# Kernel tuning notes

Hardware: AMD Instinct MI355X
Metric: run time of the kernel (lower is better)

## Reference

```python
import jax, jax.numpy as jnp
import numpy as np

# (multiplicity, irrep_dim) for irreps_in == irreps_out: 128x0e + 64x1o + 32x2e
IRREPS = [(128, 1), (64, 3), (32, 5)]
NUM_INDICES = 64
N_ELEMENTS = 8192
SCALE = 1.0  # module's `scale` arg; total coeff = scale / sqrt(num_indices) / sqrt(mul_in)
W_DIM = sum(m * m for m, _ in IRREPS)  # 21504


def setup_inputs() -> dict:
    key = jax.random.key(0)
    ks = jax.random.split(key, 5)
    x0 = jax.random.normal(ks[0], (N_ELEMENTS, 128, 1), jnp.float32)
    x1 = jax.random.normal(ks[1], (N_ELEMENTS, 64, 3), jnp.float32)
    x2 = jax.random.normal(ks[2], (N_ELEMENTS, 32, 5), jnp.float32)
    w = jax.random.normal(ks[3], (NUM_INDICES, W_DIM), jnp.float32)
    # Random contiguous segment sizes that sum exactly to N_ELEMENTS:
    bnd = jnp.sort(jax.random.randint(ks[4], (NUM_INDICES - 1,), 0, N_ELEMENTS + 1)).astype(jnp.int32)
    counts = jnp.diff(jnp.concatenate([jnp.zeros((1,), jnp.int32), bnd,
                                       jnp.full((1,), N_ELEMENTS, jnp.int32)]))
    return {"x0": x0, "x1": x1, "x2": x2, "w": w, "num_index_counts": counts}


def reference(x0, x1, x2, w, num_index_counts):
    """Indexed (segmented) equivariant linear: rows are grouped contiguously by
    num_index_counts; segment g uses weight row w[g]. Per matched irrep the
    weight block is a (mul_in, mul_out) mixing matrix applied identically to
    each of the ir.dim components (Schur's lemma), with fan-in normalization
    1/sqrt(mul_in) (cue.descriptors.linear) times scale/sqrt(num_indices)."""
    n = x0.shape[0]
    # segment id per row (rows are already grouped contiguously, as in Repeats())
    sid = jnp.repeat(jnp.arange(NUM_INDICES), num_index_counts, total_repeat_length=n)
    xs = (x0, x1, x2)
    ys = []
    off = 0
    for xk, (mul, ir_dim) in zip(xs, IRREPS):
        blk = w[:, off:off + mul * mul].reshape(NUM_INDICES, mul, mul)  # (E, m_in, m_out)
        coeff = float(SCALE / np.sqrt(NUM_INDICES) / np.sqrt(mul))
        wk = blk[sid]  # (n, m_in, m_out) per-row weight gather
        # y[n, o, i] = coeff * sum_m x[n, m, i] * w[g(n), m, o]
        ys.append(coeff * jnp.einsum('nmi,nmo->noi', xk, wk))
        off += mul * mul
    return tuple(ys)
```

## Files before the change

### kernel.cpp

```cpp
#include <hip/hip_runtime.h>

#define NSEG 64
#define NROW 8192
#define WROW 21504
#define NBPP 576
#define T0   32
#define T12  16
#define PX0  132
#define P1   196
#define P2   164
#define SBUF_FLOATS 4224

__global__ __launch_bounds__(256) void iil_kernel(
    const float* __restrict__ x0, const float* __restrict__ x1, const float* __restrict__ x2,
    const float* __restrict__ w, const int* __restrict__ counts,
    float* __restrict__ y0, float* __restrict__ y1, float* __restrict__ y2)
{
    __shared__ float sbuf[SBUF_FLOATS];
    __shared__ int sstart[NSEG + 1];
    __shared__ int t16s[NSEG + 1];
    __shared__ int t32s[NSEG + 1];

    const int t = threadIdx.x;

    if (t < NSEG) {
        int c = counts[t];
        int v = c;
        #pragma unroll
        for (int d = 1; d < NSEG; d <<= 1) {
            int u = __shfl_up(v, d, 64);
            if (t >= d) v += u;
        }
        sstart[t + 1] = v;
        int a = (c + 15) >> 4;
        #pragma unroll
        for (int d = 1; d < NSEG; d <<= 1) {
            int u = __shfl_up(a, d, 64);
            if (t >= d) a += u;
        }
        t16s[t + 1] = a;
        int b2 = (c + 31) >> 5;
        #pragma unroll
        for (int d = 1; d < NSEG; d <<= 1) {
            int u = __shfl_up(b2, d, 64);
            if (t >= d) b2 += u;
        }
        t32s[t + 1] = b2;
        if (t == 0) { sstart[0] = 0; t16s[0] = 0; t32s[0] = 0; }
    }
    __syncthreads();

    const int phase = blockIdx.x / NBPP;
    const int pb = blockIdx.x - phase * NBPP;
    const float4 z4 = make_float4(0.f, 0.f, 0.f, 0.f);

    if (phase == 0) {
        if (pb >= t32s[NSEG]) return;
        int lo = 0, hi = NSEG;
        while (hi - lo > 1) {
            int mid = (lo + hi) >> 1;
            if (t32s[mid] <= pb) lo = mid; else hi = mid;
        }
        const int g = lo;
        const int s = sstart[g] + (pb - t32s[g]) * T0;
        const int nr = min(T0, sstart[g + 1] - s);
        const float* __restrict__ wseg = w + (size_t)g * WROW;

        const float4* g0 = (const float4*)x0 + (size_t)s * 32;
        #pragma unroll
        for (int i = 0; i < 4; ++i) {
            int idx = t + i * 256;
            int r = idx >> 5, c4 = idx & 31;
            float4 v = (r < nr) ? g0[idx] : z4;
            *(float4*)(sbuf + r * PX0 + c4 * 4) = v;
        }
        __syncthreads();

        const int og = t & 31;
        const int rg = t >> 5;
        const float* wp = wseg + og * 4;
        const float* xb = sbuf + rg * 4 * PX0;
        float acc[16];
        #pragma unroll
        for (int i = 0; i < 16; ++i) acc[i] = 0.f;

        #pragma unroll 2
        for (int kq = 0; kq < 32; ++kq) {
            const int k = kq * 4;
            float4 xq0 = *(const float4*)(xb + 0 * PX0 + k);
            float4 xq1 = *(const float4*)(xb + 1 * PX0 + k);
            float4 xq2 = *(const float4*)(xb + 2 * PX0 + k);
            float4 xq3 = *(const float4*)(xb + 3 * PX0 + k);
            float4 w0q = *(const float4*)(wp + (size_t)(k + 0) * 128);
            float4 w1q = *(const float4*)(wp + (size_t)(k + 1) * 128);
            float4 w2q = *(const float4*)(wp + (size_t)(k + 2) * 128);
            float4 w3q = *(const float4*)(wp + (size_t)(k + 3) * 128);
#define RF(J, XQ)                                              \
            acc[J*4+0] = fmaf(XQ.x, w0q.x, acc[J*4+0]);        \
            acc[J*4+1] = fmaf(XQ.x, w0q.y, acc[J*4+1]);        \
            acc[J*4+2] = fmaf(XQ.x, w0q.z, acc[J*4+2]);        \
            acc[J*4+3] = fmaf(XQ.x, w0q.w, acc[J*4+3]);        \
            acc[J*4+0] = fmaf(XQ.y, w1q.x, acc[J*4+0]);        \
            acc[J*4+1] = fmaf(XQ.y, w1q.y, acc[J*4+1]);        \
            acc[J*4+2] = fmaf(XQ.y, w1q.z, acc[J*4+2]);        \
            acc[J*4+3] = fmaf(XQ.y, w1q.w, acc[J*4+3]);        \
            acc[J*4+0] = fmaf(XQ.z, w2q.x, acc[J*4+0]);        \
            acc[J*4+1] = fmaf(XQ.z, w2q.y, acc[J*4+1]);        \
            acc[J*4+2] = fmaf(XQ.z, w2q.z, acc[J*4+2]);        \
            acc[J*4+3] = fmaf(XQ.z, w2q.w, acc[J*4+3]);        \
            acc[J*4+0] = fmaf(XQ.w, w3q.x, acc[J*4+0]);        \
            acc[J*4+1] = fmaf(XQ.w, w3q.y, acc[J*4+1]);        \
            acc[J*4+2] = fmaf(XQ.w, w3q.z, acc[J*4+2]);        \
            acc[J*4+3] = fmaf(XQ.w, w3q.w, acc[J*4+3]);
            RF(0, xq0)
            RF(1, xq1)
            RF(2, xq2)
            RF(3, xq3)
#undef RF
        }
        const float c0 = 0.011048543456039806f;
        #pragma unroll
        for (int j = 0; j < 4; ++j) {
            int r = rg * 4 + j;
            if (r < nr) {
                *(float4*)(y0 + (size_t)(s + r) * 128 + og * 4) =
                    make_float4(acc[j*4+0] * c0, acc[j*4+1] * c0,
                                acc[j*4+2] * c0, acc[j*4+3] * c0);
            }
        }
    } else if (phase == 1) {
        if (pb >= t16s[NSEG]) return;
        int lo = 0, hi = NSEG;
        while (hi - lo > 1) {
            int mid = (lo + hi) >> 1;
            if (t16s[mid] <= pb) lo = mid; else hi = mid;
        }
        const int g = lo;
        const int s = sstart[g] + (pb - t16s[g]) * T12;
        const int nr = min(T12, sstart[g + 1] - s);
        const float* __restrict__ wseg = w + (size_t)g * WROW;

        float* sx1 = sbuf;
        const float4* g1 = (const float4*)x1 + (size_t)s * 48;
        #pragma unroll
        for (int i = 0; i < 3; ++i) {
            int idx = t + i * 256;
            int r = idx / 48, c = idx - r * 48;
            float4 v = (r < nr) ? g1[idx] : z4;
            *(float4*)(sx1 + r * P1 + c * 4) = v;
        }
        __syncthreads();

        const int og = t & 15;
        const int r = t >> 4;
        const float* xrow = sx1 + r * P1;
        const float* wp = wseg + 16384 + og * 4;
        float acc[12];
        #pragma unroll
        for (int i = 0; i < 12; ++i) acc[i] = 0.f;
        #pragma unroll 2
        for (int kq = 0; kq < 16; ++kq) {
            float4 xq0 = *(const float4*)(xrow + 12 * kq + 0);
            float4 xq1 = *(const float4*)(xrow + 12 * kq + 4);
            float4 xq2 = *(const float4*)(xrow + 12 * kq + 8);
            float xf[12] = {xq0.x, xq0.y, xq0.z, xq0.w,
                            xq1.x, xq1.y, xq1.z, xq1.w,
                            xq2.x, xq2.y, xq2.z, xq2.w};
            #pragma unroll
            for (int kk = 0; kk < 4; ++kk) {
                float4 wv = *(const float4*)(wp + (size_t)(4 * kq + kk) * 64);
                #pragma unroll
                for (int oo = 0; oo < 4; ++oo) {
                    float wvo = (oo == 0) ? wv.x : (oo == 1) ? wv.y : (oo == 2) ? wv.z : wv.w;
                    acc[oo * 3 + 0] = fmaf(wvo, xf[kk * 3 + 0], acc[oo * 3 + 0]);
                    acc[oo * 3 + 1] = fmaf(wvo, xf[kk * 3 + 1], acc[oo * 3 + 1]);
                    acc[oo * 3 + 2] = fmaf(wvo, xf[kk * 3 + 2], acc[oo * 3 + 2]);
                }
            }
        }
        const float c1 = 0.015625f;
        if (r < nr) {
            float* yb = y1 + (size_t)(s + r) * 192 + og * 12;
            *(float4*)(yb + 0) = make_float4(acc[0] * c1, acc[1] * c1, acc[2] * c1, acc[3] * c1);
            *(float4*)(yb + 4) = make_float4(acc[4] * c1, acc[5] * c1, acc[6] * c1, acc[7] * c1);
            *(float4*)(yb + 8) = make_float4(acc[8] * c1, acc[9] * c1, acc[10] * c1, acc[11] * c1);
        }
    } else {
        if (pb >= t16s[NSEG]) return;
        int lo = 0, hi = NSEG;
        while (hi - lo > 1) {
            int mid = (lo + hi) >> 1;
            if (t16s[mid] <= pb) lo = mid; else hi = mid;
        }
        const int g = lo;
        const int s = sstart[g] + (pb - t16s[g]) * T12;
        const int nr = min(T12, sstart[g + 1] - s);
        const float* __restrict__ wseg = w + (size_t)g * WROW;

        float* sx2 = sbuf;
        const float4* g2 = (const float4*)x2 + (size_t)s * 40;
        #pragma unroll
        for (int i = 0; i < 3; ++i) {
            int idx = t + i * 256;
            if (idx < 640) {
                int r = idx / 40, c = idx - r * 40;
                float4 v = (r < nr) ? g2[idx] : z4;
                *(float4*)(sx2 + r * P2 + c * 4) = v;
            }
        }
        __syncthreads();

        const int og = t & 15;
        const int r = t >> 4;
        const float* xrow = sx2 + r * P2;
        const float* wp = wseg + 20480 + og * 2;
        float acc[10];
        #pragma unroll
        for (int i = 0; i < 10; ++i) acc[i] = 0.f;
        #pragma unroll
        for (int kq = 0; kq < 8; ++kq) {
            float xf[20];
            #pragma unroll
            for (int j = 0; j < 5; ++j) {
                float4 v = *(const float4*)(xrow + 20 * kq + 4 * j);
                xf[4 * j + 0] = v.x; xf[4 * j + 1] = v.y; xf[4 * j + 2] = v.z; xf[4 * j + 3] = v.w;
            }
            #pragma unroll
            for (int kk = 0; kk < 4; ++kk) {
                float2 wv = *(const float2*)(wp + (size_t)(4 * kq + kk) * 32);
                #pragma unroll
                for (int i = 0; i < 5; ++i) {
                    acc[i]     = fmaf(wv.x, xf[5 * kk + i], acc[i]);
                    acc[5 + i] = fmaf(wv.y, xf[5 * kk + i], acc[5 + i]);
                }
            }
        }
        const float c2 = 0.022097086912079608f;
        if (r < nr) {
            float* yb = y2 + (size_t)(s + r) * 160 + og * 10;
            #pragma unroll
            for (int i = 0; i < 5; ++i)
                *(float2*)(yb + 2 * i) = make_float2(acc[2 * i] * c2, acc[2 * i + 1] * c2);
        }
    }
}

extern "C" void kernel_launch(void* const* d_in, const int* in_sizes, int n_in,
                              void* d_out, int out_size, void* d_ws, size_t ws_size,
                              hipStream_t stream) {
    const float* x0 = (const float*)d_in[0];
    const float* x1 = (const float*)d_in[1];
    const float* x2 = (const float*)d_in[2];
    const float* w  = (const float*)d_in[3];
    const int* counts = (const int*)d_in[4];

    float* y0 = (float*)d_out;
    float* y1 = y0 + (size_t)NROW * 128;
    float* y2 = y1 + (size_t)NROW * 192;

    hipLaunchKernelGGL(iil_kernel, dim3(3 * NBPP), dim3(256), 0, stream,
                       x0, x1, x2, w, counts, y0, y1, y2);
}
```

Measured before the change: 90.85 us.

## Software-pipeline weight loads, interleave phase blocks, set occupancy launch bound

Each phase's inner product loop now double-buffers weight (and for phase 0, shared-memory x) loads in registers, issuing the next step's global loads before computing the current step to hide latency. Block-to-phase mapping changes from contiguous ranges to round-robin (blockIdx % 3) so heavy and light phases mix across CUs. Launch bounds now request 4 blocks per SM, which may cap registers and risk spills given the doubled register buffers.

```diff
diff --git a/kernel.cpp b/kernel.cpp
--- a/kernel.cpp
+++ b/kernel.cpp
@@ -11,7 +11,7 @@
 #define P2   164
 #define SBUF_FLOATS 4224
 
-__global__ __launch_bounds__(256) void iil_kernel(
+__global__ __launch_bounds__(256, 4) void iil_kernel(
     const float* __restrict__ x0, const float* __restrict__ x1, const float* __restrict__ x2,
     const float* __restrict__ w, const int* __restrict__ counts,
     float* __restrict__ y0, float* __restrict__ y1, float* __restrict__ y2)
@@ -50,8 +50,8 @@
     }
     __syncthreads();
 
-    const int phase = blockIdx.x / NBPP;
-    const int pb = blockIdx.x - phase * NBPP;
+    const int phase = blockIdx.x % 3;
+    const int pb = blockIdx.x / 3;
     const float4 z4 = make_float4(0.f, 0.f, 0.f, 0.f);
 
     if (phase == 0) {
@@ -84,40 +84,51 @@
         #pragma unroll
         for (int i = 0; i < 16; ++i) acc[i] = 0.f;
 
-        #pragma unroll 2
-        for (int kq = 0; kq < 32; ++kq) {
-            const int k = kq * 4;
-            float4 xq0 = *(const float4*)(xb + 0 * PX0 + k);
-            float4 xq1 = *(const float4*)(xb + 1 * PX0 + k);
-            float4 xq2 = *(const float4*)(xb + 2 * PX0 + k);
-            float4 xq3 = *(const float4*)(xb + 3 * PX0 + k);
-            float4 w0q = *(const float4*)(wp + (size_t)(k + 0) * 128);
-            float4 w1q = *(const float4*)(wp + (size_t)(k + 1) * 128);
-            float4 w2q = *(const float4*)(wp + (size_t)(k + 2) * 128);
-            float4 w3q = *(const float4*)(wp + (size_t)(k + 3) * 128);
-#define RF(J, XQ)                                              \
-            acc[J*4+0] = fmaf(XQ.x, w0q.x, acc[J*4+0]);        \
-            acc[J*4+1] = fmaf(XQ.x, w0q.y, acc[J*4+1]);        \
-            acc[J*4+2] = fmaf(XQ.x, w0q.z, acc[J*4+2]);        \
-            acc[J*4+3] = fmaf(XQ.x, w0q.w, acc[J*4+3]);        \
-            acc[J*4+0] = fmaf(XQ.y, w1q.x, acc[J*4+0]);        \
-            acc[J*4+1] = fmaf(XQ.y, w1q.y, acc[J*4+1]);        \
-            acc[J*4+2] = fmaf(XQ.y, w1q.z, acc[J*4+2]);        \
-            acc[J*4+3] = fmaf(XQ.y, w1q.w, acc[J*4+3]);        \
-            acc[J*4+0] = fmaf(XQ.z, w2q.x, acc[J*4+0]);        \
-            acc[J*4+1] = fmaf(XQ.z, w2q.y, acc[J*4+1]);        \
-            acc[J*4+2] = fmaf(XQ.z, w2q.z, acc[J*4+2]);        \
-            acc[J*4+3] = fmaf(XQ.z, w2q.w, acc[J*4+3]);        \
-            acc[J*4+0] = fmaf(XQ.w, w3q.x, acc[J*4+0]);        \
-            acc[J*4+1] = fmaf(XQ.w, w3q.y, acc[J*4+1]);        \
-            acc[J*4+2] = fmaf(XQ.w, w3q.z, acc[J*4+2]);        \
-            acc[J*4+3] = fmaf(XQ.w, w3q.w, acc[J*4+3]);
-            RF(0, xq0)
-            RF(1, xq1)
-            RF(2, xq2)
-            RF(3, xq3)
-#undef RF
-        }
+        float4 wA[4], xA[4], wB[4], xB[4];
+#define LD0(WQ, XQ, KQ) do {                                      \
+            const int k_ = (KQ) * 4;                              \
+            WQ[0] = *(const float4*)(wp + (size_t)(k_ + 0) * 128);\
+            WQ[1] = *(const float4*)(wp + (size_t)(k_ + 1) * 128);\
+            WQ[2] = *(const float4*)(wp + (size_t)(k_ + 2) * 128);\
+            WQ[3] = *(const float4*)(wp + (size_t)(k_ + 3) * 128);\
+            XQ[0] = *(const float4*)(xb + 0 * PX0 + k_);          \
+            XQ[1] = *(const float4*)(xb + 1 * PX0 + k_);          \
+            XQ[2] = *(const float4*)(xb + 2 * PX0 + k_);          \
+            XQ[3] = *(const float4*)(xb + 3 * PX0 + k_);          \
+        } while (0)
+#define RF0(J, XV, WQ)                                         \
+            acc[J*4+0] = fmaf(XV.x, WQ[0].x, acc[J*4+0]);      \
+            acc[J*4+1] = fmaf(XV.x, WQ[0].y, acc[J*4+1]);      \
+            acc[J*4+2] = fmaf(XV.x, WQ[0].z, acc[J*4+2]);      \
+            acc[J*4+3] = fmaf(XV.x, WQ[0].w, acc[J*4+3]);      \
+            acc[J*4+0] = fmaf(XV.y, WQ[1].x, acc[J*4+0]);      \
+            acc[J*4+1] = fmaf(XV.y, WQ[1].y, acc[J*4+1]);      \
+            acc[J*4+2] = fmaf(XV.y, WQ[1].z, acc[J*4+2]);      \
+            acc[J*4+3] = fmaf(XV.y, WQ[1].w, acc[J*4+3]);      \
+            acc[J*4+0] = fmaf(XV.z, WQ[2].x, acc[J*4+0]);      \
+            acc[J*4+1] = fmaf(XV.z, WQ[2].y, acc[J*4+1]);      \
+            acc[J*4+2] = fmaf(XV.z, WQ[2].z, acc[J*4+2]);      \
+            acc[J*4+3] = fmaf(XV.z, WQ[2].w, acc[J*4+3]);      \
+            acc[J*4+0] = fmaf(XV.w, WQ[3].x, acc[J*4+0]);      \
+            acc[J*4+1] = fmaf(XV.w, WQ[3].y, acc[J*4+1]);      \
+            acc[J*4+2] = fmaf(XV.w, WQ[3].z, acc[J*4+2]);      \
+            acc[J*4+3] = fmaf(XV.w, WQ[3].w, acc[J*4+3]);
+#define CP0(WQ, XQ) { RF0(0, XQ[0], WQ) RF0(1, XQ[1], WQ) RF0(2, XQ[2], WQ) RF0(3, XQ[3], WQ) }
+
+        LD0(wA, xA, 0);
+        LD0(wB, xB, 1);
+        #pragma unroll 1
+        for (int kq = 0; kq < 30; kq += 2) {
+            CP0(wA, xA);
+            LD0(wA, xA, kq + 2);
+            CP0(wB, xB);
+            LD0(wB, xB, kq + 3);
+        }
+        CP0(wA, xA);
+        CP0(wB, xB);
+#undef LD0
+#undef RF0
+#undef CP0
         const float c0 = 0.011048543456039806f;
         #pragma unroll
         for (int j = 0; j < 4; ++j) {
@@ -158,26 +169,52 @@
         float acc[12];
         #pragma unroll
         for (int i = 0; i < 12; ++i) acc[i] = 0.f;
-        #pragma unroll 2
-        for (int kq = 0; kq < 16; ++kq) {
-            float4 xq0 = *(const float4*)(xrow + 12 * kq + 0);
-            float4 xq1 = *(const float4*)(xrow + 12 * kq + 4);
-            float4 xq2 = *(const float4*)(xrow + 12 * kq + 8);
-            float xf[12] = {xq0.x, xq0.y, xq0.z, xq0.w,
-                            xq1.x, xq1.y, xq1.z, xq1.w,
-                            xq2.x, xq2.y, xq2.z, xq2.w};
-            #pragma unroll
-            for (int kk = 0; kk < 4; ++kk) {
-                float4 wv = *(const float4*)(wp + (size_t)(4 * kq + kk) * 64);
-                #pragma unroll
-                for (int oo = 0; oo < 4; ++oo) {
-                    float wvo = (oo == 0) ? wv.x : (oo == 1) ? wv.y : (oo == 2) ? wv.z : wv.w;
-                    acc[oo * 3 + 0] = fmaf(wvo, xf[kk * 3 + 0], acc[oo * 3 + 0]);
-                    acc[oo * 3 + 1] = fmaf(wvo, xf[kk * 3 + 1], acc[oo * 3 + 1]);
-                    acc[oo * 3 + 2] = fmaf(wvo, xf[kk * 3 + 2], acc[oo * 3 + 2]);
-                }
-            }
-        }
+
+        float4 wA[4], wB[4];
+#define LD1(WQ, KQ) do {                                              \
+            WQ[0] = *(const float4*)(wp + (size_t)((KQ)*4 + 0) * 64); \
+            WQ[1] = *(const float4*)(wp + (size_t)((KQ)*4 + 1) * 64); \
+            WQ[2] = *(const float4*)(wp + (size_t)((KQ)*4 + 2) * 64); \
+            WQ[3] = *(const float4*)(wp + (size_t)((KQ)*4 + 3) * 64); \
+        } while (0)
+#define CP1(WQ, KQ) do {                                              \
+            float4 xq0 = *(const float4*)(xrow + 12 * (KQ) + 0);      \
+            float4 xq1 = *(const float4*)(xrow + 12 * (KQ) + 4);      \
+            float4 xq2 = *(const float4*)(xrow + 12 * (KQ) + 8);      \
+            float xf[12] = {xq0.x, xq0.y, xq0.z, xq0.w,               \
+                            xq1.x, xq1.y, xq1.z, xq1.w,               \
+                            xq2.x, xq2.y, xq2.z, xq2.w};              \
+            _Pragma("unroll")                                         \
+            for (int kk = 0; kk < 4; ++kk) {                          \
+                float4 wv = WQ[kk];                                   \
+                acc[0]  = fmaf(wv.x, xf[kk*3+0], acc[0]);             \
+                acc[1]  = fmaf(wv.x, xf[kk*3+1], acc[1]);             \
+                acc[2]  = fmaf(wv.x, xf[kk*3+2], acc[2]);             \
+                acc[3]  = fmaf(wv.y, xf[kk*3+0], acc[3]);             \
+                acc[4]  = fmaf(wv.y, xf[kk*3+1], acc[4]);             \
+                acc[5]  = fmaf(wv.y, xf[kk*3+2], acc[5]);             \
+                acc[6]  = fmaf(wv.z, xf[kk*3+0], acc[6]);             \
+                acc[7]  = fmaf(wv.z, xf[kk*3+1], acc[7]);             \
+                acc[8]  = fmaf(wv.z, xf[kk*3+2], acc[8]);             \
+                acc[9]  = fmaf(wv.w, xf[kk*3+0], acc[9]);             \
+                acc[10] = fmaf(wv.w, xf[kk*3+1], acc[10]);            \
+                acc[11] = fmaf(wv.w, xf[kk*3+2], acc[11]);            \
+            }                                                         \
+        } while (0)
+
+        LD1(wA, 0);
+        LD1(wB, 1);
+        #pragma unroll 1
+        for (int kq = 0; kq < 14; kq += 2) {
+            CP1(wA, kq);
+            LD1(wA, kq + 2);
+            CP1(wB, kq + 1);
+            LD1(wB, kq + 3);
+        }
+        CP1(wA, 14);
+        CP1(wB, 15);
+#undef LD1
+#undef CP1
         const float c1 = 0.015625f;
         if (r < nr) {
             float* yb = y1 + (size_t)(s + r) * 192 + og * 12;
@@ -217,24 +254,46 @@
         float acc[10];
         #pragma unroll
         for (int i = 0; i < 10; ++i) acc[i] = 0.f;
-        #pragma unroll
-        for (int kq = 0; kq < 8; ++kq) {
-            float xf[20];
-            #pragma unroll
-            for (int j = 0; j < 5; ++j) {
-                float4 v = *(const float4*)(xrow + 20 * kq + 4 * j);
-                xf[4 * j + 0] = v.x; xf[4 * j + 1] = v.y; xf[4 * j + 2] = v.z; xf[4 * j + 3] = v.w;
-            }
-            #pragma unroll
-            for (int kk = 0; kk < 4; ++kk) {
-                float2 wv = *(const float2*)(wp + (size_t)(4 * kq + kk) * 32);
-                #pragma unroll
-                for (int i = 0; i < 5; ++i) {
-                    acc[i]     = fmaf(wv.x, xf[5 * kk + i], acc[i]);
-                    acc[5 + i] = fmaf(wv.y, xf[5 * kk + i], acc[5 + i]);
-                }
-            }
-        }
+
+        float2 wA[4], wB[4];
+#define LD2(WQ, KQ) do {                                              \
+            WQ[0] = *(const float2*)(wp + (size_t)((KQ)*4 + 0) * 32); \
+            WQ[1] = *(const float2*)(wp + (size_t)((KQ)*4 + 1) * 32); \
+            WQ[2] = *(const float2*)(wp + (size_t)((KQ)*4 + 2) * 32); \
+            WQ[3] = *(const float2*)(wp + (size_t)((KQ)*4 + 3) * 32); \
+        } while (0)
+#define CP2(WQ, KQ) do {                                              \
+            float xf[20];                                             \
+            _Pragma("unroll")                                         \
+            for (int j = 0; j < 5; ++j) {                             \
+                float4 v = *(const float4*)(xrow + 20 * (KQ) + 4 * j);\
+                xf[4*j+0] = v.x; xf[4*j+1] = v.y;                     \
+                xf[4*j+2] = v.z; xf[4*j+3] = v.w;                     \
+            }                                                         \
+            _Pragma("unroll")                                         \
+            for (int kk = 0; kk < 4; ++kk) {                          \
+                float2 wv = WQ[kk];                                   \
+                _Pragma("unroll")                                     \
+                for (int i = 0; i < 5; ++i) {                         \
+                    acc[i]     = fmaf(wv.x, xf[5*kk+i], acc[i]);      \
+                    acc[5 + i] = fmaf(wv.y, xf[5*kk+i], acc[5 + i]);  \
+                }                                                     \
+            }                                                         \
+        } while (0)
+
+        LD2(wA, 0);
+        LD2(wB, 1);
+        #pragma unroll 1
+        for (int kq = 0; kq < 6; kq += 2) {
+            CP2(wA, kq);
+            LD2(wA, kq + 2);
+            CP2(wB, kq + 1);
+            LD2(wB, kq + 3);
+        }
+        CP2(wA, 6);
+        CP2(wB, 7);
+#undef LD2
+#undef CP2
         const float c2 = 0.022097086912079608f;
         if (r < nr) {
             float* yb = y2 + (size_t)(s + r) * 160 + og * 10;
```

Measured after the change: 92.80 us. 1.02x slower.

## Use bf16 MFMA for the scalar-irrep phase with 64-row tiles

Applied to the files above, without the earlier changes.

Phase 0 (the 128x128 scalar block) now converts x0 rows and the segment's weight block to bf16 in shared memory and computes the product with 16x16x32 bf16 MFMA instructions instead of fp32 FMAs. The tile grows from 32 to 64 rows so each block reuses the staged weights across more rows. The aim is to cut the FMA issue cost of this phase. In exchange it adds per-block weight conversion and transpose work, scalar rather than vector output stores, and bf16 rounding error that may exceed the tolerance.

```diff
diff --git a/kernel.cpp b/kernel.cpp
--- a/kernel.cpp
+++ b/kernel.cpp
@@ -1,25 +1,34 @@
 #include <hip/hip_runtime.h>
+
+typedef __attribute__((ext_vector_type(8))) short bf16x8;
+typedef __attribute__((ext_vector_type(4))) float f32x4;
 
 #define NSEG 64
 #define NROW 8192
 #define WROW 21504
 #define NBPP 576
-#define T0   32
+#define T0   64
 #define T12  16
-#define PX0  132
+#define PA   136
+#define PB   136
 #define P1   196
 #define P2   164
-#define SBUF_FLOATS 4224
+
+__device__ __forceinline__ unsigned short f2bf(float f) {
+    unsigned u = __float_as_uint(f);
+    u += 0x7fffu + ((u >> 16) & 1u);
+    return (unsigned short)(u >> 16);
+}
 
 __global__ __launch_bounds__(256) void iil_kernel(
     const float* __restrict__ x0, const float* __restrict__ x1, const float* __restrict__ x2,
     const float* __restrict__ w, const int* __restrict__ counts,
     float* __restrict__ y0, float* __restrict__ y1, float* __restrict__ y2)
 {
-    __shared__ float sbuf[SBUF_FLOATS];
+    __shared__ __align__(16) unsigned short smem_u[T0 * PA + 128 * PB];
     __shared__ int sstart[NSEG + 1];
     __shared__ int t16s[NSEG + 1];
-    __shared__ int t32s[NSEG + 1];
+    __shared__ int t64s[NSEG + 1];
 
     const int t = threadIdx.x;
 
@@ -39,93 +48,104 @@
             if (t >= d) a += u;
         }
         t16s[t + 1] = a;
-        int b2 = (c + 31) >> 5;
+        int b2 = (c + 63) >> 6;
         #pragma unroll
         for (int d = 1; d < NSEG; d <<= 1) {
             int u = __shfl_up(b2, d, 64);
             if (t >= d) b2 += u;
         }
-        t32s[t + 1] = b2;
-        if (t == 0) { sstart[0] = 0; t16s[0] = 0; t32s[0] = 0; }
+        t64s[t + 1] = b2;
+        if (t == 0) { sstart[0] = 0; t16s[0] = 0; t64s[0] = 0; }
     }
     __syncthreads();
 
     const int phase = blockIdx.x / NBPP;
     const int pb = blockIdx.x - phase * NBPP;
     const float4 z4 = make_float4(0.f, 0.f, 0.f, 0.f);
+    float* sbuf = (float*)smem_u;
 
     if (phase == 0) {
-        if (pb >= t32s[NSEG]) return;
+        if (pb >= t64s[NSEG]) return;
         int lo = 0, hi = NSEG;
         while (hi - lo > 1) {
             int mid = (lo + hi) >> 1;
-            if (t32s[mid] <= pb) lo = mid; else hi = mid;
+            if (t64s[mid] <= pb) lo = mid; else hi = mid;
         }
         const int g = lo;
-        const int s = sstart[g] + (pb - t32s[g]) * T0;
+        const int s = sstart[g] + (pb - t64s[g]) * T0;
         const int nr = min(T0, sstart[g + 1] - s);
         const float* __restrict__ wseg = w + (size_t)g * WROW;
 
+        unsigned short* As = smem_u;
+        unsigned short* Bs = smem_u + T0 * PA;
+
         const float4* g0 = (const float4*)x0 + (size_t)s * 32;
         #pragma unroll
-        for (int i = 0; i < 4; ++i) {
-            int idx = t + i * 256;
-            int r = idx >> 5, c4 = idx & 31;
+        for (int i = 0; i < 8; ++i) {
+            int idx = t + i * 256;
+            int r = idx >> 5, c4 = (idx & 31) * 4;
             float4 v = (r < nr) ? g0[idx] : z4;
-            *(float4*)(sbuf + r * PX0 + c4 * 4) = v;
+            ushort4 bv;
+            bv.x = f2bf(v.x); bv.y = f2bf(v.y); bv.z = f2bf(v.z); bv.w = f2bf(v.w);
+            *(ushort4*)(As + r * PA + c4) = bv;
+        }
+        #pragma unroll
+        for (int i = 0; i < 8; ++i) {
+            int idx = t + i * 256;
+            int k2 = idx >> 5;
+            int o4 = (idx & 31) * 4;
+            float4 va = *(const float4*)(wseg + (size_t)(2 * k2) * 128 + o4);
+            float4 vb = *(const float4*)(wseg + (size_t)(2 * k2 + 1) * 128 + o4);
+            *(ushort2*)(Bs + (size_t)(o4 + 0) * PB + 2 * k2) = make_ushort2(f2bf(va.x), f2bf(vb.x));
+            *(ushort2*)(Bs + (size_t)(o4 + 1) * PB + 2 * k2) = make_ushort2(f2bf(va.y), f2bf(vb.y));
+            *(ushort2*)(Bs + (size_t)(o4 + 2) * PB + 2 * k2) = make_ushort2(f2bf(va.z), f2bf(vb.z));
+            *(ushort2*)(Bs + (size_t)(o4 + 3) * PB + 2 * k2) = make_ushort2(f2bf(va.w), f2bf(vb.w));
         }
         __syncthreads();
 
-        const int og = t & 31;
-        const int rg = t >> 5;
-        const float* wp = wseg + og * 4;
-        const float* xb = sbuf + rg * 4 * PX0;
-        float acc[16];
-        #pragma unroll
-        for (int i = 0; i < 16; ++i) acc[i] = 0.f;
-
-        #pragma unroll 2
-        for (int kq = 0; kq < 32; ++kq) {
-            const int k = kq * 4;
-            float4 xq0 = *(const float4*)(xb + 0 * PX0 + k);
-            float4 xq1 = *(const float4*)(xb + 1 * PX0 + k);
-            float4 xq2 = *(const float4*)(xb + 2 * PX0 + k);
-            float4 xq3 = *(const float4*)(xb + 3 * PX0 + k);
-            float4 w0q = *(const float4*)(wp + (size_t)(k + 0) * 128);
-            float4 w1q = *(const float4*)(wp + (size_t)(k + 1) * 128);
-            float4 w2q = *(const float4*)(wp + (size_t)(k + 2) * 128);
-            float4 w3q = *(const float4*)(wp + (size_t)(k + 3) * 128);
-#define RF(J, XQ)                                              \
-            acc[J*4+0] = fmaf(XQ.x, w0q.x, acc[J*4+0]);        \
-            acc[J*4+1] = fmaf(XQ.x, w0q.y, acc[J*4+1]);        \
-            acc[J*4+2] = fmaf(XQ.x, w0q.z, acc[J*4+2]);        \
-            acc[J*4+3] = fmaf(XQ.x, w0q.w, acc[J*4+3]);        \
-            acc[J*4+0] = fmaf(XQ.y, w1q.x, acc[J*4+0]);        \
-            acc[J*4+1] = fmaf(XQ.y, w1q.y, acc[J*4+1]);        \
-            acc[J*4+2] = fmaf(XQ.y, w1q.z, acc[J*4+2]);        \
-            acc[J*4+3] = fmaf(XQ.y, w1q.w, acc[J*4+3]);        \
-            acc[J*4+0] = fmaf(XQ.z, w2q.x, acc[J*4+0]);        \
-            acc[J*4+1] = fmaf(XQ.z, w2q.y, acc[J*4+1]);        \
-            acc[J*4+2] = fmaf(XQ.z, w2q.z, acc[J*4+2]);        \
-            acc[J*4+3] = fmaf(XQ.z, w2q.w, acc[J*4+3]);        \
-            acc[J*4+0] = fmaf(XQ.w, w3q.x, acc[J*4+0]);        \
-            acc[J*4+1] = fmaf(XQ.w, w3q.y, acc[J*4+1]);        \
-            acc[J*4+2] = fmaf(XQ.w, w3q.z, acc[J*4+2]);        \
-            acc[J*4+3] = fmaf(XQ.w, w3q.w, acc[J*4+3]);
-            RF(0, xq0)
-            RF(1, xq1)
-            RF(2, xq2)
-            RF(3, xq3)
-#undef RF
-        }
+        const int lane = t & 63;
+        const int wv = t >> 6;
+        const int l16 = lane & 15;
+        const int quad = lane >> 4;
+        const int mp = wv & 1;
+        const int np = wv >> 1;
+
+        f32x4 acc[2][4];
+        #pragma unroll
+        for (int mt = 0; mt < 2; ++mt)
+            #pragma unroll
+            for (int nt = 0; nt < 4; ++nt)
+                acc[mt][nt] = (f32x4){0.f, 0.f, 0.f, 0.f};
+
+        const unsigned short* Abase = As + ((2 * mp) * 16 + l16) * PA + quad * 8;
+        const unsigned short* Bbase = Bs + (size_t)((4 * np) * 16 + l16) * PB + quad * 8;
+
+        #pragma unroll
+        for (int ks = 0; ks < 4; ++ks) {
+            const int ko = ks * 32;
+            bf16x8 a0 = *(const bf16x8*)(Abase + ko);
+            bf16x8 a1 = *(const bf16x8*)(Abase + 16 * PA + ko);
+            #pragma unroll
+            for (int nt = 0; nt < 4; ++nt) {
+                bf16x8 b = *(const bf16x8*)(Bbase + (size_t)nt * 16 * PB + ko);
+                acc[0][nt] = __builtin_amdgcn_mfma_f32_16x16x32_bf16(a0, b, acc[0][nt], 0, 0, 0);
+                acc[1][nt] = __builtin_amdgcn_mfma_f32_16x16x32_bf16(a1, b, acc[1][nt], 0, 0, 0);
+            }
+        }
+
         const float c0 = 0.011048543456039806f;
         #pragma unroll
-        for (int j = 0; j < 4; ++j) {
-            int r = rg * 4 + j;
-            if (r < nr) {
-                *(float4*)(y0 + (size_t)(s + r) * 128 + og * 4) =
-                    make_float4(acc[j*4+0] * c0, acc[j*4+1] * c0,
-                                acc[j*4+2] * c0, acc[j*4+3] * c0);
+        for (int mt = 0; mt < 2; ++mt) {
+            int rbase = (2 * mp + mt) * 16 + quad * 4;
+            #pragma unroll
+            for (int nt = 0; nt < 4; ++nt) {
+                int col = (4 * np + nt) * 16 + l16;
+                #pragma unroll
+                for (int rg = 0; rg < 4; ++rg) {
+                    int r = rbase + rg;
+                    if (r < nr)
+                        y0[(size_t)(s + r) * 128 + col] = acc[mt][nt][rg] * c0;
+                }
             }
         }
     } else if (phase == 1) {
```

New measurement: 95.27 us. 4.9% more time.
